# Kernel optimization log

Measured on AMD Instinct MI355X. Metric: run time of the kernel, lower is better.

The kernel has to match this reference:

```python
import jax, jax.numpy as jnp
import numpy as np

EMBED_DIM = 1024
NUM_HEADS = 16
HEAD_DIM = EMBED_DIM // NUM_HEADS
B, L = 4, 2048


def _xavier(key, out_dim, in_dim):
    limit = jnp.sqrt(6.0 / (in_dim + out_dim))
    return jax.random.uniform(key, (out_dim, in_dim), jnp.float32, -limit, limit)


def setup_inputs() -> dict:
    key = jax.random.key(0)
    kx, kq, kk, kv, ko = jax.random.split(key, 5)
    return {
        "x": jax.random.normal(kx, (B, L, EMBED_DIM), jnp.float32),
        "Wq": _xavier(kq, EMBED_DIM, EMBED_DIM), "bq": jnp.zeros((EMBED_DIM,), jnp.float32),
        "Wk": _xavier(kk, EMBED_DIM, EMBED_DIM), "bk": jnp.zeros((EMBED_DIM,), jnp.float32),
        "Wv": _xavier(kv, EMBED_DIM, EMBED_DIM), "bv": jnp.zeros((EMBED_DIM,), jnp.float32),
        "Wo": _xavier(ko, EMBED_DIM, EMBED_DIM), "bo": jnp.zeros((EMBED_DIM,), jnp.float32),
    }


def reference(x, Wq, bq, Wk, bk, Wv, bv, Wo, bo):
    bs, l, e = x.shape
    h, hd = NUM_HEADS, HEAD_DIM
    # torch Linear: y = x @ W.T + b
    q = (x @ Wq.T + bq).reshape(bs, l, h, hd).transpose(0, 2, 1, 3)  # [b,h,l,hd]
    k = (x @ Wk.T + bk).reshape(bs, l, h, hd).transpose(0, 2, 1, 3)
    v = (x @ Wv.T + bv).reshape(bs, l, h, hd).transpose(0, 2, 1, 3)
    scale = 1.0 / jnp.sqrt(jnp.asarray(hd, x.dtype))
    scores = jnp.einsum("bhqd,bhkd->bhqk", q, k) * scale  # [b,h,l,l]
    attn = jax.nn.softmax(scores, axis=-1)
    out = jnp.einsum("bhqk,bhkd->bhqd", attn, v)  # [b,h,l,hd]
    out = out.transpose(0, 2, 1, 3).reshape(bs, l, e)
    return out @ Wo.T + bo
```

## Files before the change

kernel.cpp:

```cpp
#include <hip/hip_runtime.h>
#include <hip/hip_bf16.h>
#include <stdint.h>

#define NB 4
#define NL 2048
#define NE 1024
#define NH 16
#define ND 64
#define NM (NB*NL)

typedef float f32x4 __attribute__((ext_vector_type(4)));
typedef short s16x8 __attribute__((ext_vector_type(8)));

__device__ __forceinline__ unsigned short f2b(float f) {
  uint32_t u = __float_as_uint(f);
  u += 0x7fffu + ((u >> 16) & 1u);
  return (unsigned short)(u >> 16);
}

__device__ __forceinline__ uint32_t pk2(float a, float b) {
  __hip_bfloat162 h = __float22bfloat162_rn(make_float2(a, b));
  union { __hip_bfloat162 h; uint32_t u; } c; c.h = h; return c.u;
}

__device__ __forceinline__ void gload16(const void* g, void* l) {
  __builtin_amdgcn_global_load_lds((const __attribute__((address_space(1))) void*)g,
                                   (__attribute__((address_space(3))) void*)l, 16, 0, 0);
}

__global__ void cvt_kernel(const float* __restrict__ in, unsigned short* __restrict__ out, int n8) {
  int stride = gridDim.x * blockDim.x;
  for (int i = blockIdx.x * blockDim.x + threadIdx.x; i < n8; i += stride) {
    const float4* p = (const float4*)in + (size_t)i * 2;
    float4 a = p[0], b = p[1];
    uint4 r;
    r.x = pk2(a.x, a.y); r.y = pk2(a.z, a.w);
    r.z = pk2(b.x, b.y); r.w = pk2(b.z, b.w);
    *((uint4*)out + i) = r;
  }
}

__global__ void cvt4_kernel(const float* __restrict__ w0, const float* __restrict__ w1,
                            const float* __restrict__ w2, const float* __restrict__ w3,
                            unsigned short* __restrict__ o0, unsigned short* __restrict__ o1,
                            unsigned short* __restrict__ o2, unsigned short* __restrict__ o3,
                            int n8) {
  const int y = blockIdx.y;
  const float* in = (y == 0) ? w0 : (y == 1) ? w1 : (y == 2) ? w2 : w3;
  unsigned short* out = (y == 0) ? o0 : (y == 1) ? o1 : (y == 2) ? o2 : o3;
  int stride = gridDim.x * blockDim.x;
  for (int i = blockIdx.x * blockDim.x + threadIdx.x; i < n8; i += stride) {
    const float4* p = (const float4*)in + (size_t)i * 2;
    float4 a = p[0], b = p[1];
    uint4 r;
    r.x = pk2(a.x, a.y); r.y = pk2(a.z, a.w);
    r.z = pk2(b.x, b.y); r.w = pk2(b.z, b.w);
    *((uint4*)out + i) = r;
  }
}

template<int MODE>
__launch_bounds__(256, 2)
__global__ void gemm_bt(const unsigned short* __restrict__ A,
                        const unsigned short* __restrict__ W0,
                        const unsigned short* __restrict__ W1,
                        const unsigned short* __restrict__ W2,
                        const float* __restrict__ b0,
                        const float* __restrict__ b1,
                        const float* __restrict__ b2,
                        unsigned short* __restrict__ O0,
                        unsigned short* __restrict__ O1,
                        unsigned short* __restrict__ O2,
                        float* __restrict__ fout)
{
  __shared__ alignas(16) char smem[32768];
  char* sA = smem;
  char* sB = smem + 16384;

  const int tid = threadIdx.x;
  const int lane = tid & 63;
  const int wid = tid >> 6;
  const int bx = blockIdx.x, by = blockIdx.y;
  const int m0 = by * 128;

  int which = 0;
  const unsigned short* Wsel;
  const float* bias;
  int n0;
  if (MODE == 0) {
    which = bx >> 3;
    Wsel = (which == 0) ? W0 : ((which == 1) ? W1 : W2);
    bias = (which == 0) ? b0 : ((which == 1) ? b1 : b2);
    n0 = (bx & 7) * 128;
  } else {
    Wsel = W0; bias = b0; n0 = bx * 128;
  }

  const int wr = (wid >> 1) * 64;
  const int wc = (wid & 1) * 64;
  int aaddr[4], baddr[4];
#pragma unroll
  for (int m = 0; m < 4; ++m) {
    int ra = wr + m * 16 + (lane & 15);
    aaddr[m] = ra * 128 + (((lane >> 4) * 16) ^ ((ra & 7) << 4));
    int rb = wc + m * 16 + (lane & 15);
    baddr[m] = rb * 128 + (((lane >> 4) * 16) ^ ((rb & 7) << 4));
  }

  f32x4 acc[4][4] = {};
  const int c0 = wid * 64 + lane;

  for (int kt = 0; kt < 16; ++kt) {
    const int k0 = kt * 64;
#pragma unroll
    for (int it = 0; it < 4; ++it) {
      int c = it * 256 + c0;
      int row = c >> 3;
      int sb = ((((c & 7) << 4)) ^ ((row & 7) << 4)) >> 1;
      gload16(A    + (size_t)(m0 + row) * NE + k0 + sb, sA + it * 4096 + wid * 1024);
      gload16(Wsel + (size_t)(n0 + row) * NE + k0 + sb, sB + it * 4096 + wid * 1024);
    }
    __syncthreads();
#pragma unroll
    for (int kk = 0; kk < 2; ++kk) {
      s16x8 af[4], bf[4];
#pragma unroll
      for (int m = 0; m < 4; ++m) af[m] = *(const s16x8*)(sA + (aaddr[m] ^ (kk << 6)));
#pragma unroll
      for (int n = 0; n < 4; ++n) bf[n] = *(const s16x8*)(sB + (baddr[n] ^ (kk << 6)));
#pragma unroll
      for (int m = 0; m < 4; ++m)
#pragma unroll
        for (int n = 0; n < 4; ++n)
          acc[m][n] = __builtin_amdgcn_mfma_f32_16x16x32_bf16(af[m], bf[n], acc[m][n], 0, 0, 0);
    }
    __syncthreads();
  }

  const float qsc = (MODE == 0 && ((bx >> 3) == 0)) ? 0.18033688011112042f : 1.0f;
#pragma unroll
  for (int m = 0; m < 4; ++m) {
    const int row0 = m0 + wr + m * 16 + ((lane >> 4) << 2);
#pragma unroll
    for (int n = 0; n < 4; ++n) {
      const int col = n0 + wc + n * 16 + (lane & 15);
      const float bv = bias[col];
      if (MODE == 1) {
#pragma unroll
        for (int r = 0; r < 4; ++r)
          fout[(size_t)(row0 + r) * NE + col] = acc[m][n][r] + bv;
      } else {
        const int b = row0 >> 11;
        const int l = row0 & 2047;
        const int h = col >> 6;
        const int d = col & 63;
        if (which < 2) {
          unsigned short* dst = (which == 0) ? O0 : O1;
#pragma unroll
          for (int r = 0; r < 4; ++r)
            dst[((size_t)(b * NH + h) * NL + (l + r)) * ND + d] = f2b((acc[m][n][r] + bv) * qsc);
        } else {
          uint2 w;
          w.x = pk2(acc[m][n][0] + bv, acc[m][n][1] + bv);
          w.y = pk2(acc[m][n][2] + bv, acc[m][n][3] + bv);
          *(uint2*)(O2 + ((size_t)(b * NH + h) * ND + d) * NL + l) = w;
        }
      }
    }
  }
}

__launch_bounds__(256, 3)
__global__ void attn_kernel(const unsigned short* __restrict__ Q,
                            const unsigned short* __restrict__ K,
                            const unsigned short* __restrict__ Vt,
                            unsigned short* __restrict__ AO)
{
  __shared__ alignas(16) char smem[49152];

  const int tid = threadIdx.x;
  const int lane = tid & 63;
  const int wid = tid >> 6;
  const int hi = lane >> 4;
  const int qi = lane & 15;
  const int qt = blockIdx.x;
  const int bh = blockIdx.y;
  const int b = bh >> 4;
  const int h = bh & 15;
  const size_t base = (size_t)bh * NL * ND;
  const int q0 = qt * 128 + wid * 32;

  s16x8 qf[2][2];
#pragma unroll
  for (int m = 0; m < 2; ++m)
#pragma unroll
    for (int kk = 0; kk < 2; ++kk)
      qf[m][kk] = *(const s16x8*)(Q + base + (size_t)(q0 + m * 16 + qi) * ND
                                  + kk * 32 + hi * 8);

  f32x4 o[2][4] = {};
  float rm[2] = {-1e30f, -1e30f};
  float rl[2] = {0.f, 0.f};

  int kaddr[4], vaddr[4];
#pragma unroll
  for (int n = 0; n < 4; ++n) {
    int rk = n * 16 + qi;
    kaddr[n] = rk * 128 + ((hi * 16) ^ ((rk & 7) << 4));
    vaddr[n] = kaddr[n];
  }
  char* sP = smem + 32768 + wid * 4096;
  int pwoff[4], proff[2];
#pragma unroll
  for (int n = 0; n < 4; ++n)
    pwoff[n] = qi * 128 + ((n * 32 + hi * 8) ^ ((qi & 7) << 4));
#pragma unroll
  for (int ks = 0; ks < 2; ++ks)
    proff[ks] = qi * 128 + ((ks * 64 + hi * 16) ^ ((qi & 7) << 4));

#define STAGE(T, BUF)                                                          \
  do {                                                                         \
    const int kv0_ = (T) * 64;                                                 \
    char* sKb_ = smem + (BUF) * 8192;                                          \
    char* sVb_ = smem + 16384 + (BUF) * 8192;                                  \
    _Pragma("unroll")                                                          \
    for (int it = 0; it < 2; ++it) {                                           \
      int c = it * 256 + wid * 64 + lane;                                      \
      int row = c >> 3;                                                        \
      int sb = (((c & 7) << 4) ^ ((row & 7) << 4)) >> 1;                       \
      gload16(K  + base + (size_t)(kv0_ + row) * ND + sb,                      \
              sKb_ + it * 4096 + wid * 1024);                                  \
      gload16(Vt + base + (size_t)row * NL + kv0_ + sb,                        \
              sVb_ + it * 4096 + wid * 1024);                                  \
    }                                                                          \
  } while (0)

  STAGE(0, 0);
  __syncthreads();

  for (int t = 0; t < 32; ++t) {
    const int cur = t & 1;
    if (t < 31) STAGE(t + 1, cur ^ 1);
    const char* sKb = smem + cur * 8192;
    const char* sVb = smem + 16384 + cur * 8192;

    f32x4 s[2][4] = {};
    __builtin_amdgcn_s_setprio(1);
#pragma unroll
    for (int kk = 0; kk < 2; ++kk) {
      s16x8 kf[4];
#pragma unroll
      for (int n = 0; n < 4; ++n) kf[n] = *(const s16x8*)(sKb + (kaddr[n] ^ (kk << 6)));
#pragma unroll
      for (int m = 0; m < 2; ++m)
#pragma unroll
        for (int n = 0; n < 4; ++n)
          s[m][n] = __builtin_amdgcn_mfma_f32_16x16x32_bf16(kf[n], qf[m][kk], s[m][n], 0, 0, 0);
    }
    __builtin_amdgcn_s_setprio(0);

#pragma unroll
    for (int m = 0; m < 2; ++m) {
      float a0 = fmaxf(fmaxf(fmaxf(s[m][0][0], s[m][0][1]), s[m][0][2]), s[m][0][3]);
      float a1 = fmaxf(fmaxf(fmaxf(s[m][1][0], s[m][1][1]), s[m][1][2]), s[m][1][3]);
      float a2 = fmaxf(fmaxf(fmaxf(s[m][2][0], s[m][2][1]), s[m][2][2]), s[m][2][3]);
      float a3 = fmaxf(fmaxf(fmaxf(s[m][3][0], s[m][3][1]), s[m][3][2]), s[m][3][3]);
      float pm = fmaxf(fmaxf(a0, a1), fmaxf(a2, a3));
      pm = fmaxf(pm, __shfl_xor(pm, 16));
      pm = fmaxf(pm, __shfl_xor(pm, 32));
      float mn = rm[m];
      if (!__all(pm - mn <= 8.0f)) {
        mn = fmaxf(mn, pm);
        float al = __builtin_amdgcn_exp2f(rm[m] - mn);
        rl[m] *= al;
#pragma unroll
        for (int dt = 0; dt < 4; ++dt) o[m][dt] = o[m][dt] * al;
        rm[m] = mn;
      }
      float ts = 0.f;
#pragma unroll
      for (int n = 0; n < 4; ++n) {
        float p0 = __builtin_amdgcn_exp2f(s[m][n][0] - mn);
        float p1 = __builtin_amdgcn_exp2f(s[m][n][1] - mn);
        float p2 = __builtin_amdgcn_exp2f(s[m][n][2] - mn);
        float p3 = __builtin_amdgcn_exp2f(s[m][n][3] - mn);
        ts += (p0 + p1) + (p2 + p3);
        uint2 w;
        w.x = pk2(p0, p1);
        w.y = pk2(p2, p3);
        *(uint2*)(sP + m * 2048 + pwoff[n]) = w;
      }
      ts += __shfl_xor(ts, 16);
      ts += __shfl_xor(ts, 32);
      rl[m] += ts;
    }

    __builtin_amdgcn_s_setprio(1);
#pragma unroll
    for (int ks = 0; ks < 2; ++ks) {
      s16x8 vf[4];
#pragma unroll
      for (int dt = 0; dt < 4; ++dt) vf[dt] = *(const s16x8*)(sVb + (vaddr[dt] ^ (ks << 6)));
#pragma unroll
      for (int m = 0; m < 2; ++m) {
        s16x8 pf = *(const s16x8*)(sP + m * 2048 + proff[ks]);
#pragma unroll
        for (int dt = 0; dt < 4; ++dt)
          o[m][dt] = __builtin_amdgcn_mfma_f32_16x16x32_bf16(vf[dt], pf, o[m][dt], 0, 0, 0);
      }
    }
    __builtin_amdgcn_s_setprio(0);
    __syncthreads();
  }
#undef STAGE

#pragma unroll
  for (int m = 0; m < 2; ++m) {
    const float inv = 1.0f / rl[m];
    const int qg = q0 + m * 16 + qi;
#pragma unroll
    for (int dt = 0; dt < 4; ++dt) {
      uint2 w;
      w.x = pk2(o[m][dt][0] * inv, o[m][dt][1] * inv);
      w.y = pk2(o[m][dt][2] * inv, o[m][dt][3] * inv);
      *(uint2*)(AO + (size_t)(b * NL + qg) * NE + h * 64 + dt * 16 + hi * 4) = w;
    }
  }
}

extern "C" void kernel_launch(void* const* d_in, const int* in_sizes, int n_in,
                              void* d_out, int out_size, void* d_ws, size_t ws_size,
                              hipStream_t stream) {
  const float* x  = (const float*)d_in[0];
  const float* Wq = (const float*)d_in[1];
  const float* bq = (const float*)d_in[2];
  const float* Wk = (const float*)d_in[3];
  const float* bk = (const float*)d_in[4];
  const float* Wv = (const float*)d_in[5];
  const float* bv = (const float*)d_in[6];
  const float* Wo = (const float*)d_in[7];
  const float* bo = (const float*)d_in[8];
  float* out = (float*)d_out;
  char* ws = (char*)d_ws;

  unsigned short* xb  = (unsigned short*)(ws);
  unsigned short* AOw = (unsigned short*)(ws);
  unsigned short* wqb = (unsigned short*)(ws + (16u << 20));
  unsigned short* wkb = (unsigned short*)(ws + (18u << 20));
  unsigned short* wvb = (unsigned short*)(ws + (20u << 20));
  unsigned short* wob = (unsigned short*)(ws + (22u << 20));
  unsigned short* Qw  = (unsigned short*)(ws + (24u << 20));
  unsigned short* Kw  = (unsigned short*)(ws + (40u << 20));
  unsigned short* Vtw = (unsigned short*)(ws + (56u << 20));
  (void)in_sizes; (void)n_in; (void)out_size; (void)ws_size;

  cvt_kernel<<<1024, 256, 0, stream>>>(x, xb, (NM * NE) / 8);
  cvt4_kernel<<<dim3(128, 4), 256, 0, stream>>>(Wq, Wk, Wv, Wo,
                                                wqb, wkb, wvb, wob, (NE * NE) / 8);

  gemm_bt<0><<<dim3(24, 64), 256, 0, stream>>>(xb, wqb, wkb, wvb, bq, bk, bv,
                                               Qw, Kw, Vtw, nullptr);
  attn_kernel<<<dim3(16, 64), 256, 0, stream>>>(Qw, Kw, Vtw, AOw);
  gemm_bt<1><<<dim3(8, 64), 256, 0, stream>>>(AOw, wob, nullptr, nullptr, bo,
                                              nullptr, nullptr,
                                              nullptr, nullptr, nullptr, out);
}
```

Baseline: 299.4 us.

## Switch attention to 32x32x16 MFMA and keep P in registers via lane shuffles

The attention inner loop now uses 32x32x16 bf16 MFMA tiles, so each wave handles 32 query rows with two 16-float accumulators instead of 2x4 16x16 tiles. The softmax probabilities no longer go through a per-wave LDS scratch buffer. They are repacked into the B-operand layout in registers with cross-half-wave shuffles. Dropping the P buffer shrinks shared memory from 48KB to 32KB, and launch bounds rise to 4 blocks per CU for occupancy. The risks are extra register pressure and shuffle cost, and the operand layout mapping must be exactly right.

```diff
diff --git a/kernel.cpp b/kernel.cpp
--- a/kernel.cpp
+++ b/kernel.cpp
@@ -10,7 +10,9 @@
 #define NM (NB*NL)
 
 typedef float f32x4 __attribute__((ext_vector_type(4)));
+typedef float f32x16 __attribute__((ext_vector_type(16)));
 typedef short s16x8 __attribute__((ext_vector_type(8)));
+typedef unsigned int u32x4 __attribute__((ext_vector_type(4)));
 
 __device__ __forceinline__ unsigned short f2b(float f) {
   uint32_t u = __float_as_uint(f);
@@ -170,19 +172,19 @@
   }
 }
 
-__launch_bounds__(256, 3)
+__launch_bounds__(256, 4)
 __global__ void attn_kernel(const unsigned short* __restrict__ Q,
                             const unsigned short* __restrict__ K,
                             const unsigned short* __restrict__ Vt,
                             unsigned short* __restrict__ AO)
 {
-  __shared__ alignas(16) char smem[49152];
+  __shared__ alignas(16) char smem[32768];
 
   const int tid = threadIdx.x;
   const int lane = tid & 63;
   const int wid = tid >> 6;
-  const int hi = lane >> 4;
-  const int qi = lane & 15;
+  const int ql = lane & 31;
+  const int hh = lane >> 5;
   const int qt = blockIdx.x;
   const int bh = blockIdx.y;
   const int b = bh >> 4;
@@ -190,33 +192,22 @@
   const size_t base = (size_t)bh * NL * ND;
   const int q0 = qt * 128 + wid * 32;
 
-  s16x8 qf[2][2];
-#pragma unroll
-  for (int m = 0; m < 2; ++m)
-#pragma unroll
-    for (int kk = 0; kk < 2; ++kk)
-      qf[m][kk] = *(const s16x8*)(Q + base + (size_t)(q0 + m * 16 + qi) * ND
-                                  + kk * 32 + hi * 8);
-
-  f32x4 o[2][4] = {};
-  float rm[2] = {-1e30f, -1e30f};
-  float rl[2] = {0.f, 0.f};
-
-  int kaddr[4], vaddr[4];
-#pragma unroll
-  for (int n = 0; n < 4; ++n) {
-    int rk = n * 16 + qi;
-    kaddr[n] = rk * 128 + ((hi * 16) ^ ((rk & 7) << 4));
-    vaddr[n] = kaddr[n];
-  }
-  char* sP = smem + 32768 + wid * 4096;
-  int pwoff[4], proff[2];
-#pragma unroll
-  for (int n = 0; n < 4; ++n)
-    pwoff[n] = qi * 128 + ((n * 32 + hi * 8) ^ ((qi & 7) << 4));
-#pragma unroll
-  for (int ks = 0; ks < 2; ++ks)
-    proff[ks] = qi * 128 + ((ks * 64 + hi * 16) ^ ((qi & 7) << 4));
+  s16x8 qf[4];
+#pragma unroll
+  for (int ks = 0; ks < 4; ++ks)
+    qf[ks] = *(const s16x8*)(Q + base + (size_t)(q0 + ql) * ND + ks * 16 + hh * 8);
+
+  int fa[2][4];
+#pragma unroll
+  for (int t = 0; t < 2; ++t)
+#pragma unroll
+    for (int ks = 0; ks < 4; ++ks) {
+      int r = t * 32 + ql;
+      fa[t][ks] = r * 128 + ((ks * 32 + hh * 16) ^ ((r & 7) << 4));
+    }
+
+  f32x16 o0 = {}, o1 = {};
+  float rm = -1e30f, rl = 0.f;
 
 #define STAGE(T, BUF)                                                          \
   do {                                                                         \
@@ -244,87 +235,106 @@
     const char* sKb = smem + cur * 8192;
     const char* sVb = smem + 16384 + cur * 8192;
 
-    f32x4 s[2][4] = {};
+    f32x16 s0 = {}, s1 = {};
     __builtin_amdgcn_s_setprio(1);
 #pragma unroll
-    for (int kk = 0; kk < 2; ++kk) {
-      s16x8 kf[4];
-#pragma unroll
-      for (int n = 0; n < 4; ++n) kf[n] = *(const s16x8*)(sKb + (kaddr[n] ^ (kk << 6)));
-#pragma unroll
-      for (int m = 0; m < 2; ++m)
-#pragma unroll
-        for (int n = 0; n < 4; ++n)
-          s[m][n] = __builtin_amdgcn_mfma_f32_16x16x32_bf16(kf[n], qf[m][kk], s[m][n], 0, 0, 0);
+    for (int ks = 0; ks < 4; ++ks) {
+      s16x8 kf0 = *(const s16x8*)(sKb + fa[0][ks]);
+      s16x8 kf1 = *(const s16x8*)(sKb + fa[1][ks]);
+      s0 = __builtin_amdgcn_mfma_f32_32x32x16_bf16(kf0, qf[ks], s0, 0, 0, 0);
+      s1 = __builtin_amdgcn_mfma_f32_32x32x16_bf16(kf1, qf[ks], s1, 0, 0, 0);
     }
     __builtin_amdgcn_s_setprio(0);
 
-#pragma unroll
-    for (int m = 0; m < 2; ++m) {
-      float a0 = fmaxf(fmaxf(fmaxf(s[m][0][0], s[m][0][1]), s[m][0][2]), s[m][0][3]);
-      float a1 = fmaxf(fmaxf(fmaxf(s[m][1][0], s[m][1][1]), s[m][1][2]), s[m][1][3]);
-      float a2 = fmaxf(fmaxf(fmaxf(s[m][2][0], s[m][2][1]), s[m][2][2]), s[m][2][3]);
-      float a3 = fmaxf(fmaxf(fmaxf(s[m][3][0], s[m][3][1]), s[m][3][2]), s[m][3][3]);
-      float pm = fmaxf(fmaxf(a0, a1), fmaxf(a2, a3));
-      pm = fmaxf(pm, __shfl_xor(pm, 16));
-      pm = fmaxf(pm, __shfl_xor(pm, 32));
-      float mn = rm[m];
-      if (!__all(pm - mn <= 8.0f)) {
-        mn = fmaxf(mn, pm);
-        float al = __builtin_amdgcn_exp2f(rm[m] - mn);
-        rl[m] *= al;
-#pragma unroll
-        for (int dt = 0; dt < 4; ++dt) o[m][dt] = o[m][dt] * al;
-        rm[m] = mn;
+    float q0m = fmaxf(fmaxf(s0[0], s0[1]), fmaxf(s0[2], s0[3]));
+    float q1m = fmaxf(fmaxf(s0[4], s0[5]), fmaxf(s0[6], s0[7]));
+    float q2m = fmaxf(fmaxf(s0[8], s0[9]), fmaxf(s0[10], s0[11]));
+    float q3m = fmaxf(fmaxf(s0[12], s0[13]), fmaxf(s0[14], s0[15]));
+    float q4m = fmaxf(fmaxf(s1[0], s1[1]), fmaxf(s1[2], s1[3]));
+    float q5m = fmaxf(fmaxf(s1[4], s1[5]), fmaxf(s1[6], s1[7]));
+    float q6m = fmaxf(fmaxf(s1[8], s1[9]), fmaxf(s1[10], s1[11]));
+    float q7m = fmaxf(fmaxf(s1[12], s1[13]), fmaxf(s1[14], s1[15]));
+    float pm = fmaxf(fmaxf(fmaxf(q0m, q1m), fmaxf(q2m, q3m)),
+                     fmaxf(fmaxf(q4m, q5m), fmaxf(q6m, q7m)));
+    pm = fmaxf(pm, __shfl_xor(pm, 32));
+
+    float mn = rm;
+    if (!__all(pm - mn <= 8.0f)) {
+      mn = fmaxf(mn, pm);
+      float al = __builtin_amdgcn_exp2f(rm - mn);
+      rl *= al;
+      o0 = o0 * al;
+      o1 = o1 * al;
+      rm = mn;
+    }
+
+    uint32_t w0[8], w1[8];
+    float ts0 = 0.f, ts1 = 0.f, ts2 = 0.f, ts3 = 0.f;
+#pragma unroll
+    for (int i = 0; i < 8; ++i) {
+      float e0 = __builtin_amdgcn_exp2f(s0[2 * i]     - mn);
+      float e1 = __builtin_amdgcn_exp2f(s0[2 * i + 1] - mn);
+      float e2 = __builtin_amdgcn_exp2f(s1[2 * i]     - mn);
+      float e3 = __builtin_amdgcn_exp2f(s1[2 * i + 1] - mn);
+      ts0 += e0; ts1 += e1; ts2 += e2; ts3 += e3;
+      w0[i] = pk2(e0, e1);
+      w1[i] = pk2(e2, e3);
+    }
+    float ts = (ts0 + ts1) + (ts2 + ts3);
+    ts += __shfl_xor(ts, 32);
+    rl += ts;
+
+    s16x8 pfr[4];
+#pragma unroll
+    for (int tt = 0; tt < 2; ++tt) {
+      const uint32_t* w = tt ? w1 : w0;
+      u32x4 lo, hi;
+#pragma unroll
+      for (int aa = 0; aa < 2; ++aa) {
+        uint32_t v  = hh ? w[aa] : w[aa + 2];
+        uint32_t sv = (uint32_t)__shfl_xor((int)v, 32);
+        lo[aa]     = hh ? sv        : w[aa];
+        lo[aa + 2] = hh ? w[aa + 2] : sv;
       }
-      float ts = 0.f;
-#pragma unroll
-      for (int n = 0; n < 4; ++n) {
-        float p0 = __builtin_amdgcn_exp2f(s[m][n][0] - mn);
-        float p1 = __builtin_amdgcn_exp2f(s[m][n][1] - mn);
-        float p2 = __builtin_amdgcn_exp2f(s[m][n][2] - mn);
-        float p3 = __builtin_amdgcn_exp2f(s[m][n][3] - mn);
-        ts += (p0 + p1) + (p2 + p3);
-        uint2 w;
-        w.x = pk2(p0, p1);
-        w.y = pk2(p2, p3);
-        *(uint2*)(sP + m * 2048 + pwoff[n]) = w;
+#pragma unroll
+      for (int aa = 0; aa < 2; ++aa) {
+        uint32_t v  = hh ? w[aa + 4] : w[aa + 6];
+        uint32_t sv = (uint32_t)__shfl_xor((int)v, 32);
+        hi[aa]     = hh ? sv        : w[aa + 4];
+        hi[aa + 2] = hh ? w[aa + 6] : sv;
       }
-      ts += __shfl_xor(ts, 16);
-      ts += __shfl_xor(ts, 32);
-      rl[m] += ts;
+      pfr[2 * tt]     = __builtin_bit_cast(s16x8, lo);
+      pfr[2 * tt + 1] = __builtin_bit_cast(s16x8, hi);
     }
 
     __builtin_amdgcn_s_setprio(1);
 #pragma unroll
-    for (int ks = 0; ks < 2; ++ks) {
-      s16x8 vf[4];
-#pragma unroll
-      for (int dt = 0; dt < 4; ++dt) vf[dt] = *(const s16x8*)(sVb + (vaddr[dt] ^ (ks << 6)));
-#pragma unroll
-      for (int m = 0; m < 2; ++m) {
-        s16x8 pf = *(const s16x8*)(sP + m * 2048 + proff[ks]);
-#pragma unroll
-        for (int dt = 0; dt < 4; ++dt)
-          o[m][dt] = __builtin_amdgcn_mfma_f32_16x16x32_bf16(vf[dt], pf, o[m][dt], 0, 0, 0);
-      }
+    for (int ks = 0; ks < 4; ++ks) {
+      s16x8 vf0 = *(const s16x8*)(sVb + fa[0][ks]);
+      s16x8 vf1 = *(const s16x8*)(sVb + fa[1][ks]);
+      o0 = __builtin_amdgcn_mfma_f32_32x32x16_bf16(vf0, pfr[ks], o0, 0, 0, 0);
+      o1 = __builtin_amdgcn_mfma_f32_32x32x16_bf16(vf1, pfr[ks], o1, 0, 0, 0);
     }
     __builtin_amdgcn_s_setprio(0);
     __syncthreads();
   }
 #undef STAGE
 
-#pragma unroll
-  for (int m = 0; m < 2; ++m) {
-    const float inv = 1.0f / rl[m];
-    const int qg = q0 + m * 16 + qi;
-#pragma unroll
-    for (int dt = 0; dt < 4; ++dt) {
-      uint2 w;
-      w.x = pk2(o[m][dt][0] * inv, o[m][dt][1] * inv);
-      w.y = pk2(o[m][dt][2] * inv, o[m][dt][3] * inv);
-      *(uint2*)(AO + (size_t)(b * NL + qg) * NE + h * 64 + dt * 16 + hi * 4) = w;
-    }
+  const float inv = 1.0f / rl;
+  const size_t orow = (size_t)(b * NL + q0 + ql) * NE + h * 64;
+#pragma unroll
+  for (int q4 = 0; q4 < 4; ++q4) {
+    uint2 wv;
+    wv.x = pk2(o0[4 * q4] * inv, o0[4 * q4 + 1] * inv);
+    wv.y = pk2(o0[4 * q4 + 2] * inv, o0[4 * q4 + 3] * inv);
+    *(uint2*)(AO + orow + 4 * hh + 8 * q4) = wv;
+  }
+#pragma unroll
+  for (int q4 = 0; q4 < 4; ++q4) {
+    uint2 wv;
+    wv.x = pk2(o1[4 * q4] * inv, o1[4 * q4 + 1] * inv);
+    wv.y = pk2(o1[4 * q4 + 2] * inv, o1[4 * q4 + 3] * inv);
+    *(uint2*)(AO + orow + 32 + 4 * hh + 8 * q4) = wv;
   }
 }
 
```

New measurement: 298.5 us. No clear change (-0.3%).
